# Performance work log

Measured on AMD Instinct MI355X. Metric: run time of the kernel, lower is better.

## Reference

```python
import jax, jax.numpy as jnp
import numpy as np
from jax import lax

D_MODEL, D_STATE, D_CONV, EXPAND = 192, 16, 3, 2
D_INNER = EXPAND * D_MODEL          # 384
DT_RANK = -(-D_MODEL // 16)         # 12
LN_EPS = 1e-5


def setup_inputs() -> dict:
    key = jax.random.key(0)
    ks = jax.random.split(key, 12)
    B, H, W = 4, 64, 64
    inv_sq = lambda n: 1.0 / np.sqrt(n)
    x = jax.random.normal(ks[0], (B, H, W, D_MODEL), jnp.float32)
    prompt = jax.random.normal(ks[1], (B, H, W, D_MODEL), jnp.float32)
    W_in = jax.random.normal(ks[2], (D_MODEL, 2 * D_INNER), jnp.float32) * inv_sq(D_MODEL)
    conv_w = jax.random.normal(ks[3], (D_INNER, 1, D_CONV, D_CONV), jnp.float32) * inv_sq(D_CONV * D_CONV)
    conv_b = jax.random.normal(ks[4], (D_INNER,), jnp.float32) * 0.02
    Wx = jax.random.normal(ks[5], (D_INNER, DT_RANK + 2 * D_STATE), jnp.float32) * inv_sq(D_INNER)
    Wdt = jax.random.uniform(ks[6], (DT_RANK, D_INNER), jnp.float32, -DT_RANK ** -0.5, DT_RANK ** -0.5)
    # dt bias init: inverse softplus of dt ~ LogUniform(1e-3, 0.1)
    dt = jnp.exp(jax.random.uniform(ks[7], (D_INNER,), jnp.float32) * (np.log(0.1) - np.log(1e-3)) + np.log(1e-3))
    dt = jnp.clip(dt, 1e-4, None)
    b_dt = dt + jnp.log(-jnp.expm1(-dt))
    A_log = jnp.log(jnp.broadcast_to(jnp.arange(1, D_STATE + 1, dtype=jnp.float32), (D_INNER, D_STATE)))
    D = jnp.ones((D_INNER,), jnp.float32)
    Wp = jax.random.normal(ks[8], (D_MODEL, D_STATE), jnp.float32) * inv_sq(D_MODEL)
    ln_g = jnp.ones((D_INNER,), jnp.float32)
    ln_b = jnp.zeros((D_INNER,), jnp.float32)
    Wout = jax.random.normal(ks[9], (D_INNER, D_MODEL), jnp.float32) * inv_sq(D_INNER)
    return dict(x=x, prompt=prompt, W_in=W_in, conv_w=conv_w, conv_b=conv_b, Wx=Wx,
                Wdt=Wdt, b_dt=b_dt, A_log=A_log, D=D, Wp=Wp, ln_g=ln_g, ln_b=ln_b, Wout=Wout)


def _selective_scan(u, delta, A, Bs, Cs, D):
    # u, delta: [B, L, d]; Bs, Cs: [B, L, n]; A: [d, n]; D: [d]
    Bsz = u.shape[0]
    h0 = jnp.zeros((Bsz, D_INNER, D_STATE), u.dtype)

    def step(h, inp):
        dl, uu, b, c = inp                      # [B,d],[B,d],[B,n],[B,n]
        dA = jnp.exp(dl[..., None] * A)          # [B,d,n]
        h = dA * h + (dl * uu)[..., None] * b[:, None, :]
        y = jnp.einsum('bdn,bn->bd', h, c)
        return h, y

    xs = (jnp.moveaxis(delta, 1, 0), jnp.moveaxis(u, 1, 0),
          jnp.moveaxis(Bs, 1, 0), jnp.moveaxis(Cs, 1, 0))
    _, ys = lax.scan(step, h0, xs)               # ys: [L,B,d]
    return jnp.moveaxis(ys, 0, 1) + u * D        # [B,L,d]


def reference(x, prompt, W_in, conv_w, conv_b, Wx, Wdt, b_dt, A_log, D, Wp, ln_g, ln_b, Wout):
    B, H, W, C = x.shape
    L = H * W
    xz = x @ W_in                                 # [B,H,W,2*d_inner]
    xi, z = jnp.split(xz, 2, axis=-1)
    # depthwise conv2d (NCHW, groups=d_inner)
    xc = jnp.transpose(xi, (0, 3, 1, 2))
    pad = (D_CONV - 1) // 2
    xc = lax.conv_general_dilated(xc, conv_w, (1, 1), [(pad, pad), (pad, pad)],
                                  dimension_numbers=('NCHW', 'OIHW', 'NCHW'),
                                  feature_group_count=D_INNER)
    xc = xc + conv_b[None, :, None, None]
    xc = jax.nn.silu(xc)
    u = jnp.transpose(xc.reshape(B, D_INNER, L), (0, 2, 1))   # [B,L,d]
    x_dbl = u @ Wx                                            # [B,L,r+2n]
    dtr = x_dbl[..., :DT_RANK]
    Bs = x_dbl[..., DT_RANK:DT_RANK + D_STATE]
    Cs = x_dbl[..., DT_RANK + D_STATE:]
    delta = jax.nn.softplus(dtr @ Wdt + b_dt)                 # [B,L,d] (delta_bias + softplus)
    Cs = Cs + prompt.reshape(B, L, C) @ Wp                    # prompt-conditioned C
    A = -jnp.exp(A_log)                                       # [d,n]
    y = _selective_scan(u, delta, A, Bs, Cs, D)               # [B,L,d]
    # out_norm (LayerNorm over d_inner)
    mu = jnp.mean(y, axis=-1, keepdims=True)
    var = jnp.mean(jnp.square(y - mu), axis=-1, keepdims=True)
    y = (y - mu) * lax.rsqrt(var + LN_EPS) * ln_g + ln_b
    y = y.reshape(B, H, W, D_INNER)
    y = y * jax.nn.silu(z)
    return y @ Wout
```

## Files before the change

### kernel.cpp

```cpp
#include <hip/hip_runtime.h>
#include <hip/hip_bf16.h>

#define BB 4
#define HH 64
#define WW 64
#define LL 4096
#define DM 192
#define DI 384
#define NS 16
#define RK 12
#define NC 128
#define CH 32
#define ROWS 16384
#define XDS 64
#define LOG2E 1.44269504f

typedef __bf16 bf16x8 __attribute__((ext_vector_type(8)));
typedef float  f32x4  __attribute__((ext_vector_type(4)));

#if defined(__has_builtin)
#if __has_builtin(__builtin_amdgcn_exp2f)
#define fexp2(x) __builtin_amdgcn_exp2f(x)
#else
#define fexp2(x) exp2f(x)
#endif
#else
#define fexp2(x) exp2f(x)
#endif

__device__ __forceinline__ float fsilu(float x) {
    return x / (1.0f + __expf(-x));
}

__device__ __forceinline__ unsigned short f2bf(float f) {
    unsigned int u = __float_as_uint(f);
    unsigned int r = (u + 0x7fffu + ((u >> 16) & 1u)) >> 16;
    return (unsigned short)r;
}

__global__ __launch_bounds__(256) void f32_to_bf16_vec(
    const float* __restrict__ src, unsigned short* __restrict__ dst, int n4)
{
    int i = blockIdx.x * 256 + threadIdx.x;
    if (i < n4) {
        float4 v = ((const float4*)src)[i];
        ((ushort4*)dst)[i] = make_ushort4(f2bf(v.x), f2bf(v.y), f2bf(v.z), f2bf(v.w));
    }
}

__global__ __launch_bounds__(256) void build_bt(
    const float* __restrict__ src, unsigned short* __restrict__ dst,
    int K, int Nsrc, int Nrows)
{
    int idx = blockIdx.x * 256 + threadIdx.x;
    if (idx >= Nrows * K) return;
    int n = idx / K, k = idx % K;
    dst[idx] = (n < Nsrc) ? f2bf(src[k * Nsrc + n]) : (unsigned short)0;
}

template<bool SPLIT>
__global__ __launch_bounds__(256) void gemm_bf16_mfma(
    const unsigned short* __restrict__ A, const unsigned short* __restrict__ BT,
    float* __restrict__ C0, float* __restrict__ C1,
    int M, int N, int K, int halfN)
{
    __shared__ __align__(16) char lds[64 * 80 * 2];
    char* As = lds;
    char* Bs = lds + 64 * 80;
    const int tid = threadIdx.x;
    const int w = tid >> 6, lane = tid & 63;
    const int wm = w >> 1, wn = w & 1;
    const int row0 = blockIdx.x * 64, col0 = blockIdx.y * 64;
    const int r = tid >> 2, cch = tid & 3;
    const int l15 = lane & 15, k8 = lane >> 4;

    f32x4 acc[2][2] = {};
    for (int k0 = 0; k0 < K; k0 += 32) {
        *(float4*)(As + r * 80 + cch * 16) =
            *(const float4*)(A + (size_t)(row0 + r) * K + k0 + cch * 8);
        *(float4*)(Bs + r * 80 + cch * 16) =
            *(const float4*)(BT + (size_t)(col0 + r) * K + k0 + cch * 8);
        __syncthreads();
        bf16x8 a0 = *(const bf16x8*)(As + (wm * 32 +      l15) * 80 + k8 * 16);
        bf16x8 a1 = *(const bf16x8*)(As + (wm * 32 + 16 + l15) * 80 + k8 * 16);
        bf16x8 b0 = *(const bf16x8*)(Bs + (wn * 32 +      l15) * 80 + k8 * 16);
        bf16x8 b1 = *(const bf16x8*)(Bs + (wn * 32 + 16 + l15) * 80 + k8 * 16);
        acc[0][0] = __builtin_amdgcn_mfma_f32_16x16x32_bf16(a0, b0, acc[0][0], 0, 0, 0);
        acc[0][1] = __builtin_amdgcn_mfma_f32_16x16x32_bf16(a0, b1, acc[0][1], 0, 0, 0);
        acc[1][0] = __builtin_amdgcn_mfma_f32_16x16x32_bf16(a1, b0, acc[1][0], 0, 0, 0);
        acc[1][1] = __builtin_amdgcn_mfma_f32_16x16x32_bf16(a1, b1, acc[1][1], 0, 0, 0);
        __syncthreads();
    }

    float* Cw;
    int cbase, cstride;
    if (SPLIT) {
        cstride = halfN;
        if (col0 < halfN) { Cw = C0; cbase = col0; }
        else              { Cw = C1; cbase = col0 - halfN; }
    } else {
        Cw = C0; cbase = col0; cstride = N;
    }
    #pragma unroll
    for (int fm = 0; fm < 2; ++fm)
        #pragma unroll
        for (int fn = 0; fn < 2; ++fn)
            #pragma unroll
            for (int reg = 0; reg < 4; ++reg) {
                int row = row0 + wm * 32 + fm * 16 + k8 * 4 + reg;
                int col = cbase + wn * 32 + fn * 16 + l15;
                Cw[(size_t)row * cstride + col] = acc[fm][fn][reg];
            }
}

__global__ __launch_bounds__(256) void conv_dw_silu(
    const float* __restrict__ xi, const float* __restrict__ conv_w,
    const float* __restrict__ conv_b, float* __restrict__ u,
    unsigned short* __restrict__ u_bf)
{
    int idx = blockIdx.x * 256 + threadIdx.x;
    int c4 = idx % 96;
    int rest = idx / 96;
    int w = rest % WW; rest /= WW;
    int h = rest % HH;
    int b = rest / HH;
    int c = c4 * 4;

    float wgt[4][9];
    #pragma unroll
    for (int q = 0; q < 4; ++q)
        #pragma unroll
        for (int t = 0; t < 9; ++t)
            wgt[q][t] = conv_w[(c + q) * 9 + t];

    float4 acc = *(const float4*)&conv_b[c];
    #pragma unroll
    for (int kh = 0; kh < 3; ++kh) {
        int hh = h + kh - 1;
        if ((unsigned)hh >= HH) continue;
        #pragma unroll
        for (int kw = 0; kw < 3; ++kw) {
            int ww = w + kw - 1;
            if ((unsigned)ww >= WW) continue;
            const float4 xv = *(const float4*)&xi[(((size_t)(b * HH + hh)) * WW + ww) * DI + c];
            int t = kh * 3 + kw;
            acc.x += xv.x * wgt[0][t];
            acc.y += xv.y * wgt[1][t];
            acc.z += xv.z * wgt[2][t];
            acc.w += xv.w * wgt[3][t];
        }
    }
    acc.x = fsilu(acc.x); acc.y = fsilu(acc.y);
    acc.z = fsilu(acc.z); acc.w = fsilu(acc.w);
    size_t off = (((size_t)b * LL) + h * WW + w) * DI + c;
    *(float4*)&u[off] = acc;
    *(ushort4*)&u_bf[off] = make_ushort4(f2bf(acc.x), f2bf(acc.y), f2bf(acc.z), f2bf(acc.w));
}

__global__ __launch_bounds__(256) void post_proj(
    const float* __restrict__ xdbl, const float* __restrict__ prompt,
    const float* __restrict__ Wdt, const float* __restrict__ b_dt,
    const float* __restrict__ Wp,
    float* __restrict__ delta, float* __restrict__ Csv)
{
    const int wid = threadIdx.x >> 6, lane = threadIdx.x & 63;
    const int row = blockIdx.x * 4 + wid;

    const float4* dp = (const float4*)&xdbl[(size_t)row * XDS];
    const float4 d0 = dp[0], d1 = dp[1], d2 = dp[2];
    const float dtr[RK] = {d0.x, d0.y, d0.z, d0.w, d1.x, d1.y, d1.z, d1.w,
                           d2.x, d2.y, d2.z, d2.w};

    const int n16 = lane & 15, g = lane >> 4;
    const float* prow = prompt + (size_t)row * DM + g * 48;
    float pw = 0.f;
    #pragma unroll
    for (int cc = 0; cc < 48; cc += 4) {
        const float4 p4 = *(const float4*)&prow[cc];
        const int c = g * 48 + cc;
        pw += p4.x * Wp[(c    ) * NS + n16];
        pw += p4.y * Wp[(c + 1) * NS + n16];
        pw += p4.z * Wp[(c + 2) * NS + n16];
        pw += p4.w * Wp[(c + 3) * NS + n16];
    }
    pw += __shfl_xor(pw, 16);
    pw += __shfl_xor(pw, 32);
    if (lane < 16)
        Csv[(size_t)row * NS + lane] = xdbl[(size_t)row * XDS + 28 + lane] + pw;

    #pragma unroll
    for (int jj = 0; jj < 6; ++jj) {
        int dch = jj * 64 + lane;
        float acc = b_dt[dch];
        #pragma unroll
        for (int r = 0; r < RK; ++r) acc += dtr[r] * Wdt[r * DI + dch];
        delta[(size_t)row * DI + dch] = (acc > 20.f) ? acc : log1pf(__expf(acc));
    }
}

__global__ __launch_bounds__(256) void scan_p1_v3(
    const float* __restrict__ delta, const float* __restrict__ u,
    const float* __restrict__ xdbl, const float* __restrict__ A_log,
    float* __restrict__ Aprod, float* __restrict__ Hout)
{
    const int g = blockIdx.x * 256 + threadIdx.x;
    const int d = g % DI;
    const int bc = g / DI;
    const int b = bc / NC, c = bc % NC;

    float Adn[NS], h[NS], ap[NS];
    #pragma unroll
    for (int n = 0; n < NS; ++n) {
        Adn[n] = -__expf(A_log[d * NS + n]) * LOG2E;
        h[n] = 0.f;
        ap[n] = 1.f;
    }
    const size_t rbase = (size_t)(b * LL + c * CH);
    const float* dp = delta + rbase * DI + d;
    const float* up = u     + rbase * DI + d;
    const float* xp = xdbl  + rbase * XDS + 12;

    float dlt = dp[0], uu = up[0];
    float4 bb0 = *(const float4*)(xp + 0), bb1 = *(const float4*)(xp + 4);
    float4 bb2 = *(const float4*)(xp + 8), bb3 = *(const float4*)(xp + 12);

    for (int i = 0; i < CH; ++i) {
        const float dlt_n = dp[(i + 1) * DI];
        const float uu_n  = up[(i + 1) * DI];
        const float* xn = xp + (i + 1) * XDS;
        const float4 bn0 = *(const float4*)(xn + 0), bn1 = *(const float4*)(xn + 4);
        const float4 bn2 = *(const float4*)(xn + 8), bn3 = *(const float4*)(xn + 12);

        const float du = dlt * uu;
        const float bs[NS] = {bb0.x, bb0.y, bb0.z, bb0.w, bb1.x, bb1.y, bb1.z, bb1.w,
                              bb2.x, bb2.y, bb2.z, bb2.w, bb3.x, bb3.y, bb3.z, bb3.w};
        #pragma unroll
        for (int n = 0; n < NS; ++n) {
            const float a = fexp2(dlt * Adn[n]);
            h[n] = a * h[n] + du * bs[n];
            ap[n] *= a;
        }
        dlt = dlt_n; uu = uu_n;
        bb0 = bn0; bb1 = bn1; bb2 = bn2; bb3 = bn3;
    }
    const size_t idx = ((size_t)bc * DI + d) * NS;
    #pragma unroll
    for (int q = 0; q < 4; ++q) {
        *(float4*)&Aprod[idx + q * 4] =
            make_float4(ap[q*4], ap[q*4+1], ap[q*4+2], ap[q*4+3]);
        *(float4*)&Hout[idx + q * 4] =
            make_float4(h[q*4], h[q*4+1], h[q*4+2], h[q*4+3]);
    }
}

__global__ __launch_bounds__(256) void scan_p2(
    float* __restrict__ Aprod, const float* __restrict__ Hout)
{
    const int gid = blockIdx.x * 256 + threadIdx.x;
    const int dn = gid % (DI * NS);
    const int b  = gid / (DI * NS);
    const size_t base = (size_t)b * NC * DI * NS + dn;
    const size_t cstride = (size_t)DI * NS;

    float hin = 0.f;
    float ap = Aprod[base], ho = Hout[base];
    for (int c = 0; c < NC; ++c) {
        const size_t idx = base + (size_t)c * cstride;
        const float ap_n = Aprod[idx + cstride];
        const float ho_n = Hout[idx + cstride];
        Aprod[idx] = hin;
        hin = ap * hin + ho;
        ap = ap_n; ho = ho_n;
    }
}

__global__ __launch_bounds__(384) void scan_p3_ln(
    const float* __restrict__ delta, const float* __restrict__ u,
    const float* __restrict__ xdbl, const float* __restrict__ Csv,
    const float* __restrict__ Hin, const float* __restrict__ A_log,
    const float* __restrict__ Dvec, const float* __restrict__ z,
    const float* __restrict__ ln_g, const float* __restrict__ ln_b,
    unsigned short* __restrict__ yin_bf)
{
    __shared__ float red_s[2][8], red_sq[2][8];
    const int d = threadIdx.x;
    const int bc = blockIdx.x;
    const int b = bc / NC, c = bc % NC;
    const int wid = d >> 6, lane = d & 63;

    float Adn[NS], h[NS];
    #pragma unroll
    for (int n = 0; n < NS; ++n)
        Adn[n] = -__expf(A_log[d * NS + n]) * LOG2E;
    {
        const size_t idx = ((size_t)bc * DI + d) * NS;
        #pragma unroll
        for (int q = 0; q < 4; ++q) {
            const float4 hv = *(const float4*)&Hin[idx + q * 4];
            h[q*4] = hv.x; h[q*4+1] = hv.y; h[q*4+2] = hv.z; h[q*4+3] = hv.w;
        }
    }
    const float Dd = Dvec[d];
    const float lg = ln_g[d], lb = ln_b[d];

    const size_t rbase = (size_t)(b * LL + c * CH);
    const float* dp = delta + rbase * DI + d;
    const float* up = u     + rbase * DI + d;
    const float* zp = z     + rbase * DI + d;
    const float* xp = xdbl  + rbase * XDS + 12;
    const float* cp = Csv   + rbase * NS;
    unsigned short* yp = yin_bf + rbase * DI + d;

    float dlt = dp[0], uu = up[0], zz = zp[0];
    float4 bb0 = *(const float4*)(xp + 0), bb1 = *(const float4*)(xp + 4);
    float4 bb2 = *(const float4*)(xp + 8), bb3 = *(const float4*)(xp + 12);
    float4 cc0 = *(const float4*)(cp + 0), cc1 = *(const float4*)(cp + 4);
    float4 cc2 = *(const float4*)(cp + 8), cc3 = *(const float4*)(cp + 12);

    for (int i = 0; i < CH; ++i) {
        const float dlt_n = dp[(i + 1) * DI];
        const float uu_n  = up[(i + 1) * DI];
        const float zz_n  = zp[(i + 1) * DI];
        const float* xn = xp + (i + 1) * XDS;
        const float* cn = cp + (i + 1) * NS;
        const float4 bn0 = *(const float4*)(xn + 0), bn1 = *(const float4*)(xn + 4);
        const float4 bn2 = *(const float4*)(xn + 8), bn3 = *(const float4*)(xn + 12);
        const float4 cn0 = *(const float4*)(cn + 0), cn1 = *(const float4*)(cn + 4);
        const float4 cn2 = *(const float4*)(cn + 8), cn3 = *(const float4*)(cn + 12);

        const float du = dlt * uu;
        const float bs[NS] = {bb0.x, bb0.y, bb0.z, bb0.w, bb1.x, bb1.y, bb1.z, bb1.w,
                              bb2.x, bb2.y, bb2.z, bb2.w, bb3.x, bb3.y, bb3.z, bb3.w};
        const float cs[NS] = {cc0.x, cc0.y, cc0.z, cc0.w, cc1.x, cc1.y, cc1.z, cc1.w,
                              cc2.x, cc2.y, cc2.z, cc2.w, cc3.x, cc3.y, cc3.z, cc3.w};
        float acc = uu * Dd;
        #pragma unroll
        for (int n = 0; n < NS; ++n) {
            const float a = fexp2(dlt * Adn[n]);
            h[n] = a * h[n] + du * bs[n];
            acc += h[n] * cs[n];
        }
        float s = acc, sq = acc * acc;
        #pragma unroll
        for (int m = 1; m < 64; m <<= 1) {
            s  += __shfl_xor(s, m);
            sq += __shfl_xor(sq, m);
        }
        const int par = i & 1;
        if (lane == 0) { red_s[par][wid] = s; red_sq[par][wid] = sq; }
        __syncthreads();
        s = red_s[par][0] + red_s[par][1] + red_s[par][2]
          + red_s[par][3] + red_s[par][4] + red_s[par][5];
        sq = red_sq[par][0] + red_sq[par][1] + red_sq[par][2]
           + red_sq[par][3] + red_sq[par][4] + red_sq[par][5];
        const float mu = s * (1.f / DI);
        const float var = sq * (1.f / DI) - mu * mu;
        const float inv = rsqrtf(var + 1e-5f);
        const float yn = (acc - mu) * inv * lg + lb;
        yp[(size_t)i * DI] = f2bf(yn * fsilu(zz));

        dlt = dlt_n; uu = uu_n; zz = zz_n;
        bb0 = bn0; bb1 = bn1; bb2 = bn2; bb3 = bn3;
        cc0 = cn0; cc1 = cn1; cc2 = cn2; cc3 = cn3;
    }
}

extern "C" void kernel_launch(void* const* d_in, const int* in_sizes, int n_in,
                              void* d_out, int out_size, void* d_ws, size_t ws_size,
                              hipStream_t stream)
{
    const float* x      = (const float*)d_in[0];
    const float* prompt = (const float*)d_in[1];
    const float* W_in   = (const float*)d_in[2];
    const float* conv_w = (const float*)d_in[3];
    const float* conv_b = (const float*)d_in[4];
    const float* Wx     = (const float*)d_in[5];
    const float* Wdt    = (const float*)d_in[6];
    const float* b_dt   = (const float*)d_in[7];
    const float* A_log  = (const float*)d_in[8];
    const float* Dvec   = (const float*)d_in[9];
    const float* Wp     = (const float*)d_in[10];
    const float* ln_g   = (const float*)d_in[11];
    const float* ln_b   = (const float*)d_in[12];
    const float* Wout   = (const float*)d_in[13];
    float* out = (float*)d_out;

    char* ws = (char*)d_ws;
    const size_t SZ_BLD = (size_t)ROWS * DI * 4;
    float* xi    = (float*)(ws);
    float* z     = (float*)(ws + SZ_BLD);
    float* u     = (float*)(ws + 2 * SZ_BLD);
    float* delta = (float*)(ws + 3 * SZ_BLD);
    char*  p     = ws + 4 * SZ_BLD;
    unsigned short* x_bf   = (unsigned short*)p;  p += (size_t)ROWS * DM * 2;
    unsigned short* u_bf   = (unsigned short*)p;  p += (size_t)ROWS * DI * 2;
    float* xdbl  = (float*)p;            p += (size_t)ROWS * XDS * 4;
    float* Csv   = (float*)p;            p += (size_t)ROWS * NS * 4;
    float* Aprod = (float*)p;            p += (size_t)BB * NC * DI * NS * 4;
    float* Hout  = (float*)p;            p += (size_t)BB * NC * DI * NS * 4;
    unsigned short* WinT   = (unsigned short*)p;  p += (size_t)(2 * DI) * DM * 2;
    unsigned short* WxPadT = (unsigned short*)p;  p += (size_t)XDS * DI * 2;
    unsigned short* WoutT  = (unsigned short*)p;  p += (size_t)DM * DI * 2;
    unsigned short* yin_bf = (unsigned short*)xi;

    f32_to_bf16_vec<<<(ROWS * DM / 4 + 255) / 256, 256, 0, stream>>>(x, x_bf, ROWS * DM / 4);
    build_bt<<<(2 * DI * DM + 255) / 256, 256, 0, stream>>>(W_in, WinT, DM, 2 * DI, 2 * DI);
    build_bt<<<(XDS * DI + 255) / 256, 256, 0, stream>>>(Wx, WxPadT, DI, 44, XDS);
    build_bt<<<(DM * DI + 255) / 256, 256, 0, stream>>>(Wout, WoutT, DI, DM, DM);

    {
        dim3 g(ROWS / 64, (2 * DI) / 64);
        gemm_bf16_mfma<true><<<g, 256, 0, stream>>>(x_bf, WinT, xi, z, ROWS, 2 * DI, DM, DI);
    }
    conv_dw_silu<<<(BB * HH * WW * 96) / 256, 256, 0, stream>>>(xi, conv_w, conv_b, u, u_bf);
    {
        dim3 g(ROWS / 64, 1);
        gemm_bf16_mfma<false><<<g, 256, 0, stream>>>(u_bf, WxPadT, xdbl, nullptr, ROWS, XDS, DI, 0);
    }
    post_proj<<<ROWS / 4, 256, 0, stream>>>(xdbl, prompt, Wdt, b_dt, Wp, delta, Csv);
    scan_p1_v3<<<(BB * NC * DI) / 256, 256, 0, stream>>>(delta, u, xdbl, A_log, Aprod, Hout);
    scan_p2<<<(BB * DI * NS) / 256, 256, 0, stream>>>(Aprod, Hout);
    scan_p3_ln<<<BB * NC, 384, 0, stream>>>(delta, u, xdbl, Csv, Aprod, A_log,
                                            Dvec, z, ln_g, ln_b, yin_bf);
    {
        dim3 g(ROWS / 64, DM / 64);
        gemm_bf16_mfma<false><<<g, 256, 0, stream>>>(yin_bf, WoutT, out, nullptr, ROWS, DM, DI, 0);
    }
}
```

Before: 288.1 us.

## Halve scan chunk length, compute chunk decay from summed delta, interleave A/H buffers

Doubles the number of scan chunks (chunk length 32 to 16) to give the chunked scan more parallelism. The per-step running product of decays is replaced by one exp2 of the summed delta per state at chunk end. Aprod and Hout are merged into one interleaved float2 buffer, and the serial pass-2 loop keeps a four-deep prefetch buffer. The bf16 staging buffers now alias the AH region to save workspace, but doubling NC also doubles pass-2 serial length and the pass-1/pass-2 traffic.

```diff
diff --git a/kernel.cpp b/kernel.cpp
--- a/kernel.cpp
+++ b/kernel.cpp
@@ -9,8 +9,8 @@
 #define DI 384
 #define NS 16
 #define RK 12
-#define NC 128
-#define CH 32
+#define NC 256
+#define CH 16
 #define ROWS 16384
 #define XDS 64
 #define LOG2E 1.44269504f
@@ -198,23 +198,31 @@
     }
 }
 
-__global__ __launch_bounds__(256) void scan_p1_v3(
+__global__ __launch_bounds__(256) void scan_p1_v4(
     const float* __restrict__ delta, const float* __restrict__ u,
     const float* __restrict__ xdbl, const float* __restrict__ A_log,
-    float* __restrict__ Aprod, float* __restrict__ Hout)
+    float* __restrict__ AH)
 {
     const int g = blockIdx.x * 256 + threadIdx.x;
     const int d = g % DI;
     const int bc = g / DI;
     const int b = bc / NC, c = bc % NC;
 
-    float Adn[NS], h[NS], ap[NS];
-    #pragma unroll
-    for (int n = 0; n < NS; ++n) {
-        Adn[n] = -__expf(A_log[d * NS + n]) * LOG2E;
-        h[n] = 0.f;
-        ap[n] = 1.f;
-    }
+    float Adn[NS], h[NS];
+    {
+        const float4* ap4 = (const float4*)(A_log + d * NS);
+        #pragma unroll
+        for (int q = 0; q < 4; ++q) {
+            const float4 v = ap4[q];
+            Adn[q*4+0] = -__expf(v.x) * LOG2E;
+            Adn[q*4+1] = -__expf(v.y) * LOG2E;
+            Adn[q*4+2] = -__expf(v.z) * LOG2E;
+            Adn[q*4+3] = -__expf(v.w) * LOG2E;
+        }
+    }
+    #pragma unroll
+    for (int n = 0; n < NS; ++n) h[n] = 0.f;
+
     const size_t rbase = (size_t)(b * LL + c * CH);
     const float* dp = delta + rbase * DI + d;
     const float* up = u     + rbase * DI + d;
@@ -223,6 +231,7 @@
     float dlt = dp[0], uu = up[0];
     float4 bb0 = *(const float4*)(xp + 0), bb1 = *(const float4*)(xp + 4);
     float4 bb2 = *(const float4*)(xp + 8), bb3 = *(const float4*)(xp + 12);
+    float sdlt = 0.f;
 
     for (int i = 0; i < CH; ++i) {
         const float dlt_n = dp[(i + 1) * DI];
@@ -232,52 +241,56 @@
         const float4 bn2 = *(const float4*)(xn + 8), bn3 = *(const float4*)(xn + 12);
 
         const float du = dlt * uu;
+        sdlt += dlt;
         const float bs[NS] = {bb0.x, bb0.y, bb0.z, bb0.w, bb1.x, bb1.y, bb1.z, bb1.w,
                               bb2.x, bb2.y, bb2.z, bb2.w, bb3.x, bb3.y, bb3.z, bb3.w};
         #pragma unroll
         for (int n = 0; n < NS; ++n) {
             const float a = fexp2(dlt * Adn[n]);
             h[n] = a * h[n] + du * bs[n];
-            ap[n] *= a;
         }
         dlt = dlt_n; uu = uu_n;
         bb0 = bn0; bb1 = bn1; bb2 = bn2; bb3 = bn3;
     }
-    const size_t idx = ((size_t)bc * DI + d) * NS;
-    #pragma unroll
-    for (int q = 0; q < 4; ++q) {
-        *(float4*)&Aprod[idx + q * 4] =
-            make_float4(ap[q*4], ap[q*4+1], ap[q*4+2], ap[q*4+3]);
-        *(float4*)&Hout[idx + q * 4] =
-            make_float4(h[q*4], h[q*4+1], h[q*4+2], h[q*4+3]);
-    }
-}
-
-__global__ __launch_bounds__(256) void scan_p2(
-    float* __restrict__ Aprod, const float* __restrict__ Hout)
+    float* dst = AH + 2 * (((size_t)bc * DI + d) * NS);
+    #pragma unroll
+    for (int q = 0; q < 8; ++q) {
+        const float ap0 = fexp2(sdlt * Adn[2*q]);
+        const float ap1 = fexp2(sdlt * Adn[2*q+1]);
+        *(float4*)(dst + 4 * q) = make_float4(ap0, h[2*q], ap1, h[2*q+1]);
+    }
+}
+
+__global__ __launch_bounds__(256) void scan_p2(float2* __restrict__ AH)
 {
     const int gid = blockIdx.x * 256 + threadIdx.x;
     const int dn = gid % (DI * NS);
     const int b  = gid / (DI * NS);
     const size_t base = (size_t)b * NC * DI * NS + dn;
-    const size_t cstride = (size_t)DI * NS;
+    const size_t cs = (size_t)DI * NS;
+
+    float2 buf[4];
+    #pragma unroll
+    for (int k = 0; k < 4; ++k) buf[k] = AH[base + (size_t)k * cs];
 
     float hin = 0.f;
-    float ap = Aprod[base], ho = Hout[base];
-    for (int c = 0; c < NC; ++c) {
-        const size_t idx = base + (size_t)c * cstride;
-        const float ap_n = Aprod[idx + cstride];
-        const float ho_n = Hout[idx + cstride];
-        Aprod[idx] = hin;
-        hin = ap * hin + ho;
-        ap = ap_n; ho = ho_n;
+    for (int c = 0; c < NC; c += 4) {
+        #pragma unroll
+        for (int k = 0; k < 4; ++k) {
+            const int cn = (c + k + 4 < NC) ? (c + k + 4) : (NC - 1);
+            const float2 nxt = AH[base + (size_t)cn * cs];
+            const float2 cur = buf[k];
+            AH[base + (size_t)(c + k) * cs].x = hin;
+            hin = cur.x * hin + cur.y;
+            buf[k] = nxt;
+        }
     }
 }
 
 __global__ __launch_bounds__(384) void scan_p3_ln(
     const float* __restrict__ delta, const float* __restrict__ u,
     const float* __restrict__ xdbl, const float* __restrict__ Csv,
-    const float* __restrict__ Hin, const float* __restrict__ A_log,
+    const float* __restrict__ AH, const float* __restrict__ A_log,
     const float* __restrict__ Dvec, const float* __restrict__ z,
     const float* __restrict__ ln_g, const float* __restrict__ ln_b,
     unsigned short* __restrict__ yin_bf)
@@ -289,15 +302,23 @@
     const int wid = d >> 6, lane = d & 63;
 
     float Adn[NS], h[NS];
-    #pragma unroll
-    for (int n = 0; n < NS; ++n)
-        Adn[n] = -__expf(A_log[d * NS + n]) * LOG2E;
-    {
-        const size_t idx = ((size_t)bc * DI + d) * NS;
+    {
+        const float4* ap4 = (const float4*)(A_log + d * NS);
         #pragma unroll
         for (int q = 0; q < 4; ++q) {
-            const float4 hv = *(const float4*)&Hin[idx + q * 4];
-            h[q*4] = hv.x; h[q*4+1] = hv.y; h[q*4+2] = hv.z; h[q*4+3] = hv.w;
+            const float4 v = ap4[q];
+            Adn[q*4+0] = -__expf(v.x) * LOG2E;
+            Adn[q*4+1] = -__expf(v.y) * LOG2E;
+            Adn[q*4+2] = -__expf(v.z) * LOG2E;
+            Adn[q*4+3] = -__expf(v.w) * LOG2E;
+        }
+    }
+    {
+        const float* hp = AH + 2 * (((size_t)bc * DI + d) * NS);
+        #pragma unroll
+        for (int q = 0; q < 8; ++q) {
+            const float4 v = *(const float4*)(hp + 4 * q);
+            h[2*q] = v.x; h[2*q+1] = v.z;
         }
     }
     const float Dd = Dvec[d];
@@ -392,15 +413,15 @@
     float* u     = (float*)(ws + 2 * SZ_BLD);
     float* delta = (float*)(ws + 3 * SZ_BLD);
     char*  p     = ws + 4 * SZ_BLD;
-    unsigned short* x_bf   = (unsigned short*)p;  p += (size_t)ROWS * DM * 2;
-    unsigned short* u_bf   = (unsigned short*)p;  p += (size_t)ROWS * DI * 2;
     float* xdbl  = (float*)p;            p += (size_t)ROWS * XDS * 4;
     float* Csv   = (float*)p;            p += (size_t)ROWS * NS * 4;
-    float* Aprod = (float*)p;            p += (size_t)BB * NC * DI * NS * 4;
-    float* Hout  = (float*)p;            p += (size_t)BB * NC * DI * NS * 4;
+    char*  ahreg = p;
+    float* AH    = (float*)p;            p += (size_t)BB * NC * DI * NS * 8;
     unsigned short* WinT   = (unsigned short*)p;  p += (size_t)(2 * DI) * DM * 2;
     unsigned short* WxPadT = (unsigned short*)p;  p += (size_t)XDS * DI * 2;
     unsigned short* WoutT  = (unsigned short*)p;  p += (size_t)DM * DI * 2;
+    unsigned short* x_bf   = (unsigned short*)ahreg;
+    unsigned short* u_bf   = (unsigned short*)(ahreg + (size_t)ROWS * DM * 2);
     unsigned short* yin_bf = (unsigned short*)xi;
 
     f32_to_bf16_vec<<<(ROWS * DM / 4 + 255) / 256, 256, 0, stream>>>(x, x_bf, ROWS * DM / 4);
@@ -418,9 +439,9 @@
         gemm_bf16_mfma<false><<<g, 256, 0, stream>>>(u_bf, WxPadT, xdbl, nullptr, ROWS, XDS, DI, 0);
     }
     post_proj<<<ROWS / 4, 256, 0, stream>>>(xdbl, prompt, Wdt, b_dt, Wp, delta, Csv);
-    scan_p1_v3<<<(BB * NC * DI) / 256, 256, 0, stream>>>(delta, u, xdbl, A_log, Aprod, Hout);
-    scan_p2<<<(BB * DI * NS) / 256, 256, 0, stream>>>(Aprod, Hout);
-    scan_p3_ln<<<BB * NC, 384, 0, stream>>>(delta, u, xdbl, Csv, Aprod, A_log,
+    scan_p1_v4<<<(BB * NC * DI) / 256, 256, 0, stream>>>(delta, u, xdbl, A_log, AH);
+    scan_p2<<<(BB * DI * NS) / 256, 256, 0, stream>>>((float2*)AH);
+    scan_p3_ln<<<BB * NC, 384, 0, stream>>>(delta, u, xdbl, Csv, AH, A_log,
                                             Dvec, z, ln_g, ln_b, yin_bf);
     {
         dim3 g(ROWS / 64, DM / 64);
```

After: 290.0 us. About the same (+0.7%).
